# Performance work log

Hardware: AMD Instinct MI355X
Metric: run time of the kernel (lower is better)

Reference implementation:

```python
import jax, jax.numpy as jnp
import numpy as np

H = 224
W = 224

def setup_inputs() -> dict:
    key = jax.random.key(0)
    x = jax.random.normal(key, (128, H, W, 5), dtype=jnp.float32)
    return {"x": x}

def reference(x):
    # Split channels: RGB image + flow fields dx, dy
    img = x[..., :3]            # [B,H,W,3]
    dx = x[..., 3]              # [B,H,W]
    dy = x[..., 4]              # [B,H,W]
    B = x.shape[0]

    # tf.meshgrid default 'xy' indexing: X varies along columns, Y along rows
    cols = jnp.arange(W, dtype=jnp.float32)
    rows = jnp.arange(H, dtype=jnp.float32)
    X = jnp.broadcast_to(cols[None, :], (H, W))   # X[i,j] = j
    Y = jnp.broadcast_to(rows[:, None], (H, W))   # Y[i,j] = i

    # Modular wrap, then truncate to int (values in [0,W) so trunc == floor)
    Xi = ((X[None] + dx) % W).astype(jnp.int32)   # [B,H,W]
    Yi = ((Y[None] + dy) % H).astype(jnp.int32)   # [B,H,W]

    # "Simple bilinear": average of 4 corner-shifted crops, then zero-pad back to HxW
    tl = img[:, 0:H-2, 0:W-2, :]
    tr = img[:, 0:H-2, 2:W,   :]
    bl = img[:, 2:H,   0:W-2, :]
    br = img[:, 2:H,   2:W,   :]
    sb = (tl + tr + bl + br) * 0.25               # [B,H-2,W-2,3]
    sbp = jnp.pad(sb, ((0, 0), (1, 1), (1, 1), (0, 0)))  # [B,H,W,3]

    # Vectorized per-batch gather: out[b,i,j,:] = sbp[b, Yi[b,i,j], Xi[b,i,j], :]
    b_idx = jnp.arange(B)[:, None, None]
    out = sbp[b_idx, Yi, Xi]                      # [B,H,W,3]
    return out
```

## Files before the change

### kernel.cpp

```cpp
#include <hip/hip_runtime.h>

#define HH 224
#define WW 224
#define NXCD 8
#define PPT 4

__global__ __launch_bounds__(256) void bilinear_gather_kernel(
    const float* __restrict__ x, float* __restrict__ out,
    int total, int nwg) {
    int p = blockIdx.x;
    int xcd = p % NXCD;
    int idx = p / NXCD;
    int q = nwg / NXCD;
    int r = nwg % NXCD;
    int lb = (xcd < r ? xcd * (q + 1) : r * (q + 1) + (xcd - r) * q) + idx;

    int base = lb * (PPT * 256) + threadIdx.x;

    float res[3 * PPT];

#pragma unroll
    for (int k = 0; k < PPT; ++k) {
        int i = base + k * 256;
        int px = i % WW;
        int t  = i / WW;
        int py = t % HH;
        int b  = t / HH;

        const float* pix = x + (size_t)i * 5;
        float dx = pix[3];
        float dy = pix[4];

        float rx = fmodf((float)px + dx, (float)WW);
        if (rx < 0.f) rx += (float)WW;
        float ry = fmodf((float)py + dy, (float)HH);
        if (ry < 0.f) ry += (float)HH;

        int xi = (int)rx; if (xi > WW - 1) xi = WW - 1;
        int yi = (int)ry; if (yi > HH - 1) yi = HH - 1;

        float m = (xi >= 1 && xi <= WW - 2 && yi >= 1 && yi <= HH - 2) ? 0.25f : 0.f;
        int xc = xi < 1 ? 1 : (xi > WW - 2 ? WW - 2 : xi);
        int yc = yi < 1 ? 1 : (yi > HH - 2 ? HH - 2 : yi);

        const float* bb = x + (size_t)b * HH * WW * 5;
        const float* p00 = bb + ((size_t)(yc - 1) * WW + (xc - 1)) * 5;
        const float* p01 = bb + ((size_t)(yc - 1) * WW + (xc + 1)) * 5;
        const float* p10 = bb + ((size_t)(yc + 1) * WW + (xc - 1)) * 5;
        const float* p11 = bb + ((size_t)(yc + 1) * WW + (xc + 1)) * 5;
        res[k * 3 + 0] = m * (p00[0] + p01[0] + p10[0] + p11[0]);
        res[k * 3 + 1] = m * (p00[1] + p01[1] + p10[1] + p11[1]);
        res[k * 3 + 2] = m * (p00[2] + p01[2] + p10[2] + p11[2]);
    }

#pragma unroll
    for (int k = 0; k < PPT; ++k) {
        int i = base + k * 256;
        float* o = out + (size_t)i * 3;
        o[0] = res[k * 3 + 0];
        o[1] = res[k * 3 + 1];
        o[2] = res[k * 3 + 2];
    }
}

extern "C" void kernel_launch(void* const* d_in, const int* in_sizes, int n_in,
                              void* d_out, int out_size, void* d_ws, size_t ws_size,
                              hipStream_t stream) {
    const float* x = (const float*)d_in[0];
    float* out = (float*)d_out;
    int total = in_sizes[0] / 5;
    int blocks = total / (PPT * 256);
    bilinear_gather_kernel<<<blocks, 256, 0, stream>>>(x, out, total, blocks);
}
```

Before: 48.15 us.

## Stage halo-padded RGB row tiles in LDS and gather from shared memory

Each workgroup now handles 8 image rows. It cooperatively loads those rows plus a 7-row wrapped halo, keeping only the RGB channels in LDS, then runs the 4-corner gather from LDS. Any lookup that lands outside the staged rows falls back to a global-memory read. The aim is to replace scattered global corner reads with LDS accesses. The cost is redundant staging of halo rows and roughly 59 KB of LDS per block, which limits occupancy, plus a barrier between the load and compute phases.

```diff
diff --git a/kernel.cpp b/kernel.cpp
--- a/kernel.cpp
+++ b/kernel.cpp
@@ -3,39 +3,67 @@
 #define HH 224
 #define WW 224
 #define NXCD 8
+#define RB 8
+#define SROWS (RB + 14)
+#define NT 448
 #define PPT 4
+#define ROWF (WW * 3)
 
-__global__ __launch_bounds__(256) void bilinear_gather_kernel(
-    const float* __restrict__ x, float* __restrict__ out,
-    int total, int nwg) {
+__global__ __launch_bounds__(NT) void bilinear_lds_kernel(
+    const float* __restrict__ x, float* __restrict__ out, int nwg) {
+    __shared__ float rgb[SROWS][ROWF];
+
     int p = blockIdx.x;
-    int xcd = p % NXCD;
-    int idx = p / NXCD;
-    int q = nwg / NXCD;
-    int r = nwg % NXCD;
+    int xcd = p % NXCD, idx = p / NXCD;
+    int q = nwg / NXCD, r = nwg % NXCD;
     int lb = (xcd < r ? xcd * (q + 1) : r * (q + 1) + (xcd - r) * q) + idx;
 
-    int base = lb * (PPT * 256) + threadIdx.x;
+    int img = lb / (HH / RB);
+    int rg  = lb % (HH / RB);
+    int y0  = rg * RB;
+    const float* base = x + (size_t)img * HH * WW * 5;
 
-    float res[3 * PPT];
+    int t = threadIdx.x;
+
+    float dxv[PPT], dyv[PPT];
+#pragma unroll
+    for (int k = 0; k < PPT; ++k) {
+        int pp = k * NT + t;
+        const float* pix = base + ((size_t)y0 * WW + pp) * 5;
+        dxv[k] = pix[3];
+        dyv[k] = pix[4];
+    }
+
+    for (int j = t; j < SROWS * 280; j += NT) {
+        int row = j / 280;
+        int c4  = j - row * 280;
+        int g = y0 - 7 + row;
+        g = (g + HH) % HH;
+        float4 v = *(const float4*)(base + (size_t)g * WW * 5 + c4 * 4);
+        int f0 = c4 * 4;
+        int px = f0 / 5;
+        int ch = f0 - px * 5;
+        float vv[4] = {v.x, v.y, v.z, v.w};
+#pragma unroll
+        for (int c = 0; c < 4; ++c) {
+            if (ch < 3) rgb[row][px * 3 + ch] = vv[c];
+            ++ch;
+            if (ch == 5) { ch = 0; ++px; }
+        }
+    }
+    __syncthreads();
 
 #pragma unroll
     for (int k = 0; k < PPT; ++k) {
-        int i = base + k * 256;
-        int px = i % WW;
-        int t  = i / WW;
-        int py = t % HH;
-        int b  = t / HH;
+        int pp = k * NT + t;
+        int prow = pp / WW;
+        int pcol = pp - prow * WW;
+        int py = y0 + prow;
 
-        const float* pix = x + (size_t)i * 5;
-        float dx = pix[3];
-        float dy = pix[4];
-
-        float rx = fmodf((float)px + dx, (float)WW);
+        float rx = fmodf((float)pcol + dxv[k], (float)WW);
         if (rx < 0.f) rx += (float)WW;
-        float ry = fmodf((float)py + dy, (float)HH);
+        float ry = fmodf((float)py + dyv[k], (float)HH);
         if (ry < 0.f) ry += (float)HH;
-
         int xi = (int)rx; if (xi > WW - 1) xi = WW - 1;
         int yi = (int)ry; if (yi > HH - 1) yi = HH - 1;
 
@@ -43,23 +71,28 @@
         int xc = xi < 1 ? 1 : (xi > WW - 2 ? WW - 2 : xi);
         int yc = yi < 1 ? 1 : (yi > HH - 2 ? HH - 2 : yi);
 
-        const float* bb = x + (size_t)b * HH * WW * 5;
-        const float* p00 = bb + ((size_t)(yc - 1) * WW + (xc - 1)) * 5;
-        const float* p01 = bb + ((size_t)(yc - 1) * WW + (xc + 1)) * 5;
-        const float* p10 = bb + ((size_t)(yc + 1) * WW + (xc - 1)) * 5;
-        const float* p11 = bb + ((size_t)(yc + 1) * WW + (xc + 1)) * 5;
-        res[k * 3 + 0] = m * (p00[0] + p01[0] + p10[0] + p11[0]);
-        res[k * 3 + 1] = m * (p00[1] + p01[1] + p10[1] + p11[1]);
-        res[k * 3 + 2] = m * (p00[2] + p01[2] + p10[2] + p11[2]);
-    }
+        int s = yc - (y0 - 7);
+        s = (s % HH + HH) % HH;
 
-#pragma unroll
-    for (int k = 0; k < PPT; ++k) {
-        int i = base + k * 256;
-        float* o = out + (size_t)i * 3;
-        o[0] = res[k * 3 + 0];
-        o[1] = res[k * 3 + 1];
-        o[2] = res[k * 3 + 2];
+        float r0, g0, b0;
+        if (s >= 1 && s <= SROWS - 2) {
+            int cm = (xc - 1) * 3, cp = (xc + 1) * 3;
+            r0 = rgb[s - 1][cm]     + rgb[s - 1][cp]     + rgb[s + 1][cm]     + rgb[s + 1][cp];
+            g0 = rgb[s - 1][cm + 1] + rgb[s - 1][cp + 1] + rgb[s + 1][cm + 1] + rgb[s + 1][cp + 1];
+            b0 = rgb[s - 1][cm + 2] + rgb[s - 1][cp + 2] + rgb[s + 1][cm + 2] + rgb[s + 1][cp + 2];
+        } else {
+            const float* p00 = base + ((size_t)(yc - 1) * WW + (xc - 1)) * 5;
+            const float* p01 = base + ((size_t)(yc - 1) * WW + (xc + 1)) * 5;
+            const float* p10 = base + ((size_t)(yc + 1) * WW + (xc - 1)) * 5;
+            const float* p11 = base + ((size_t)(yc + 1) * WW + (xc + 1)) * 5;
+            r0 = p00[0] + p01[0] + p10[0] + p11[0];
+            g0 = p00[1] + p01[1] + p10[1] + p11[1];
+            b0 = p00[2] + p01[2] + p10[2] + p11[2];
+        }
+        float* o = out + ((size_t)img * HH * WW + (size_t)y0 * WW + pp) * 3;
+        o[0] = m * r0;
+        o[1] = m * g0;
+        o[2] = m * b0;
     }
 }
 
@@ -68,7 +101,7 @@
                               hipStream_t stream) {
     const float* x = (const float*)d_in[0];
     float* out = (float*)d_out;
-    int total = in_sizes[0] / 5;
-    int blocks = total / (PPT * 256);
-    bilinear_gather_kernel<<<blocks, 256, 0, stream>>>(x, out, total, blocks);
+    int B = in_sizes[0] / (HH * WW * 5);
+    int blocks = B * (HH / RB);
+    bilinear_lds_kernel<<<blocks, NT, 0, stream>>>(x, out, blocks);
 }
```

Result: slower. 78.05 us (+62.1%).
